# Kernel tuning notes

Measured on AMD Instinct MI355X. Metric: run time of the kernel, lower is better.

The kernel has to match this reference:

```python
import jax, jax.numpy as jnp
import numpy as np

PE_SIZE = 16          # sqrt(num_patches=256)
HIDDEN_STRIDE = 2
CUBIC_A = -0.75       # torch bicubic coefficient


def cubic_resize_matrix(in_size, out_size, a=CUBIC_A):
    """(out_size, in_size) weights for torch bicubic, align_corners=False."""
    dst = np.arange(out_size)
    src = (dst + 0.5) * in_size / out_size - 0.5
    x0 = np.floor(src).astype(np.int64)
    W = np.zeros((out_size, in_size), np.float32)
    for k in range(-1, 3):  # 4 taps
        idx = np.clip(x0 + k, 0, in_size - 1)  # border replicate
        d = np.abs(src - (x0 + k))
        w = np.where(d <= 1.0, (a + 2) * d**3 - (a + 3) * d**2 + 1.0,
            np.where(d < 2.0, a * d**3 - 5 * a * d**2 + 8 * a * d - 4 * a, 0.0))
        np.add.at(W, (dst, idx), w.astype(np.float32))
    return W


def setup_inputs() -> dict:
    key = jax.random.key(0)
    k1, k2, k3, k4 = jax.random.split(key, 4)
    n_img, t, h, w = 8, 1, 64, 64
    total = n_img * t * h * w  # 32768 patches
    in_feat, d = 3 * 14 * 14, 1152
    return {
        "pixel_values": jax.random.normal(k1, (total, in_feat), jnp.float32),
        "w_patch": jax.random.normal(k2, (d, in_feat), jnp.float32) * 0.02,
        "b_patch": jax.random.normal(k3, (d,), jnp.float32) * 0.02,
        "pos_table": jax.random.normal(k4, (PE_SIZE * PE_SIZE, d), jnp.float32) * 0.02,
        "grid_thws": jnp.array([[t, h, w]] * n_img, jnp.int64),
    }


def _pos_embed(pos_table, grid):
    """grid: np int array (n_img, 3) -> (sum t*h*w, d) positional embeddings."""
    d = pos_table.shape[-1]
    pe_grid = pos_table.reshape(PE_SIZE, PE_SIZE, d)  # (H, W, d)
    s = HIDDEN_STRIDE
    pieces = []
    for t, h, w in grid:
        Wh = jnp.asarray(cubic_resize_matrix(PE_SIZE, int(h)))
        Ww = jnp.asarray(cubic_resize_matrix(PE_SIZE, int(w)))
        pe = jnp.einsum('hH,wW,HWd->hwd', Wh, Ww, pe_grid)  # (h, w, d)
        # hidden_stride window rearrange: (h,w,d) -> (h/s, w/s, s, s, d)
        pe = pe.reshape(h // s, s, w // s, s, d).transpose(0, 2, 1, 3, 4)
        pe = pe.reshape(h * w, d)
        pe = jnp.tile(pe, (int(t), 1))  # repeat over temporal dim
        pieces.append(pe)
    return jnp.concatenate(pieces, axis=0)


def reference(pixel_values, w_patch, b_patch, pos_table, grid_thws):
    # patch embedding (Linear)
    patch_embeds = pixel_values @ w_patch.T + b_patch  # (N, d)
    grid = np.asarray(grid_thws)  # static shapes per image
    pos = _pos_embed(pos_table, grid)
    return patch_embeds + pos
```

## Files before the change

### kernel.cpp

```cpp
#include <hip/hip_runtime.h>

typedef unsigned short ushort_t;
typedef unsigned int uint_t;

typedef __bf16 bf16x8 __attribute__((ext_vector_type(8)));
typedef float f32x4 __attribute__((ext_vector_type(4)));

#define KK 588
#define KP 608
#define NN 1152
#define MM 32768
#define POSROWS 4096


__device__ __forceinline__ ushort_t f2bf(float f) {
    union { float f; uint_t u; } v; v.f = f;
    uint_t u = v.u;
    uint_t r = (u + 0x7FFFu + ((u >> 16) & 1u)) >> 16;
    return (ushort_t)r;
}

__device__ __forceinline__ void cubic_taps(int dst, float* w, int* idx) {
    const float A = -0.75f;
    float src = (float)dst * 0.25f - 0.25f;
    int x0 = (int)floorf(src);
    #pragma unroll
    for (int k = -1; k <= 2; ++k) {
        int i = x0 + k;
        int ic = i < 0 ? 0 : (i > 15 ? 15 : i);
        float d = fabsf(src - (float)i);
        float wt;
        if (d <= 1.0f)      wt = ((A + 2.0f) * d - (A + 3.0f)) * d * d + 1.0f;
        else if (d < 2.0f)  wt = ((A * d - 5.0f * A) * d + 8.0f * A) * d - 4.0f * A;
        else                wt = 0.0f;
        w[k + 1] = wt;
        idx[k + 1] = ic;
    }
}


__global__ void pos_kernel(const float* __restrict__ pt, float* __restrict__ pos) {
    int n = blockIdx.x;
    int h = ((n >> 7) << 1) | ((n >> 1) & 1);
    int w = (((n >> 2) & 31) << 1) | (n & 1);
    float wh[4], ww[4];
    int ih[4], iw[4];
    cubic_taps(h, wh, ih);
    cubic_taps(w, ww, iw);
    for (int j = threadIdx.x; j < NN; j += blockDim.x) {
        float s = 0.f;
        #pragma unroll
        for (int a = 0; a < 4; ++a) {
            float rs = 0.f;
            #pragma unroll
            for (int b = 0; b < 4; ++b)
                rs += ww[b] * pt[(ih[a] * 16 + iw[b]) * NN + j];
            s += wh[a] * rs;
        }
        pos[(size_t)n * NN + j] = s;
    }
}


__global__ void cvt_pad_kernel(const float* __restrict__ src, ushort_t* __restrict__ dst,
                               int rows) {
    int idx = blockIdx.x * 256 + threadIdx.x;
    int total = rows * KP;
    if (idx >= total) return;
    int row = idx / KP;
    int k = idx - row * KP;
    float v = (k < KK) ? src[(size_t)row * KK + k] : 0.0f;
    dst[idx] = f2bf(v);
}


__global__ void gemm_kernel(const ushort_t* __restrict__ Abf,
                            const ushort_t* __restrict__ Bbf,
                            const float* __restrict__ bias,
                            const float* __restrict__ pos,
                            float* __restrict__ out) {
    __shared__ __align__(16) ushort_t lA[128 * 32];
    __shared__ __align__(16) ushort_t lB[128 * 32];

    const int t = threadIdx.x;
    const int lane = t & 63;
    const int wid = t >> 6;
    const int wm = wid >> 1, wn = wid & 1;

    const int bm = (int)blockIdx.x * 128;
    const int bn = (int)blockIdx.y * 128;

    f32x4 acc[4][4] = {};

    for (int ks = 0; ks < KP / 32; ++ks) {
        const int k0 = ks * 32;
        #pragma unroll
        for (int i = 0; i < 2; ++i) {
            int idx = i * 256 + t;
            int row = idx >> 2;
            int slot = idx & 3;
            int khi = slot ^ ((row >> 1) & 3);
            const ushort_t* gA = Abf + (size_t)(bm + row) * KP + k0 + khi * 8;
            const ushort_t* gB = Bbf + (size_t)(bn + row) * KP + k0 + khi * 8;
            ushort_t* lAp = lA + (size_t)(idx & ~63) * 8;
            ushort_t* lBp = lB + (size_t)(idx & ~63) * 8;
            __builtin_amdgcn_global_load_lds(
                (const __attribute__((address_space(1))) void*)gA,
                (__attribute__((address_space(3))) void*)lAp, 16, 0, 0);
            __builtin_amdgcn_global_load_lds(
                (const __attribute__((address_space(1))) void*)gB,
                (__attribute__((address_space(3))) void*)lBp, 16, 0, 0);
        }
        __syncthreads();

        bf16x8 af[4], bfr[4];
        #pragma unroll
        for (int mi = 0; mi < 4; ++mi) {
            int row = wm * 64 + mi * 16 + (lane & 15);
            int slot = (lane >> 4) ^ ((row >> 1) & 3);
            af[mi] = *(const bf16x8*)(lA + row * 32 + slot * 8);
        }
        #pragma unroll
        for (int ni = 0; ni < 4; ++ni) {
            int row = wn * 64 + ni * 16 + (lane & 15);
            int slot = (lane >> 4) ^ ((row >> 1) & 3);
            bfr[ni] = *(const bf16x8*)(lB + row * 32 + slot * 8);
        }
        #pragma unroll
        for (int mi = 0; mi < 4; ++mi)
            #pragma unroll
            for (int ni = 0; ni < 4; ++ni)
                acc[mi][ni] = __builtin_amdgcn_mfma_f32_16x16x32_bf16(
                    af[mi], bfr[ni], acc[mi][ni], 0, 0, 0);
        __syncthreads();
    }

    #pragma unroll
    for (int mi = 0; mi < 4; ++mi) {
        #pragma unroll
        for (int ni = 0; ni < 4; ++ni) {
            int col = bn + wn * 64 + ni * 16 + (lane & 15);
            float bcol = bias[col];
            #pragma unroll
            for (int r = 0; r < 4; ++r) {
                int row = bm + wm * 64 + mi * 16 + (lane >> 4) * 4 + r;
                int prow = row & (POSROWS - 1);
                out[(size_t)row * NN + col] =
                    acc[mi][ni][r] + bcol + pos[(size_t)prow * NN + col];
            }
        }
    }
}


__global__ void fb_kernel(const float* __restrict__ A, const float* __restrict__ W,
                          const float* __restrict__ bias, const float* __restrict__ pt,
                          float* __restrict__ out) {
    __shared__ float sA[16][17], sB[16][17];
    int ty = threadIdx.y, tx = threadIdx.x;
    int row = blockIdx.y * 16 + ty;
    int col = blockIdx.x * 16 + tx;
    float acc = 0.f;
    for (int k0 = 0; k0 < KK; k0 += 16) {
        int ka = k0 + tx;
        sA[ty][tx] = (ka < KK) ? A[(size_t)row * KK + ka] : 0.f;
        sB[ty][tx] = (ka < KK) ? W[(size_t)(blockIdx.x * 16 + ty) * KK + ka] : 0.f;
        __syncthreads();
        #pragma unroll
        for (int kk = 0; kk < 16; ++kk)
            acc += sA[ty][kk] * sB[tx][kk];
        __syncthreads();
    }
    int n = row & (POSROWS - 1);
    int h = ((n >> 7) << 1) | ((n >> 1) & 1);
    int w = (((n >> 2) & 31) << 1) | (n & 1);
    float wh[4], ww[4]; int ih[4], iw[4];
    cubic_taps(h, wh, ih);
    cubic_taps(w, ww, iw);
    float p = 0.f;
    #pragma unroll
    for (int a = 0; a < 4; ++a) {
        float rs = 0.f;
        #pragma unroll
        for (int b = 0; b < 4; ++b)
            rs += ww[b] * pt[(ih[a] * 16 + iw[b]) * NN + col];
        p += wh[a] * rs;
    }
    out[(size_t)row * NN + col] = acc + bias[col] + p;
}


extern "C" void kernel_launch(void* const* d_in, const int* in_sizes, int n_in,
                              void* d_out, int out_size, void* d_ws, size_t ws_size,
                              hipStream_t stream) {
    const float* pv   = (const float*)d_in[0];
    const float* wp   = (const float*)d_in[1];
    const float* bias = (const float*)d_in[2];
    const float* pt   = (const float*)d_in[3];
    float* out = (float*)d_out;

    const size_t pos_bytes = (size_t)POSROWS * NN * 4;
    const size_t pvb_bytes = (size_t)MM * KP * 2;
    const size_t wb_bytes  = (size_t)NN * KP * 2;
    const size_t need = pos_bytes + pvb_bytes + wb_bytes;

    if (ws_size >= need) {
        float* pos = (float*)d_ws;
        ushort_t* pvb = (ushort_t*)((char*)d_ws + pos_bytes);
        ushort_t* wb  = (ushort_t*)((char*)d_ws + pos_bytes + pvb_bytes);

        pos_kernel<<<POSROWS, 256, 0, stream>>>(pt, pos);

        int tot_pv = MM * KP;
        cvt_pad_kernel<<<(tot_pv + 255) / 256, 256, 0, stream>>>(pv, pvb, MM);
        int tot_w = NN * KP;
        cvt_pad_kernel<<<(tot_w + 255) / 256, 256, 0, stream>>>(wp, wb, NN);

        gemm_kernel<<<dim3(MM / 128, NN / 128), 256, 0, stream>>>(pvb, wb, bias, pos, out);
    } else {
        fb_kernel<<<dim3(NN / 16, MM / 16), dim3(16, 16), 0, stream>>>(pv, wp, bias, pt, out);
    }
}
```

Measured before the change: 141.6 us.

## Triple-buffer GEMM loads, remap tiles per XCD, vectorize pos and conversion kernels

The GEMM now keeps three LDS buffers and prefetches two K-steps ahead, using explicit vmcnt waits and raw barriers so global-to-LDS loads overlap the MFMA work. Workgroups are remapped to a 1D grid so that consecutive tiles land on the same XCD for L2 reuse. The pos kernel uses float4 loads with one thread per four columns, and the fp32-to-bf16 pad conversion handles 8 elements per thread with vector loads and stores. This costs three times the LDS per block, which may lower occupancy, and the hand-written wait counts depend on exactly four loads being issued per stage.

Measured after the change: 131.9 us. -6.9%, faster.

```diff
diff --git a/kernel.cpp b/kernel.cpp
--- a/kernel.cpp
+++ b/kernel.cpp
@@ -11,14 +11,10 @@
 #define NN 1152
 #define MM 32768
 #define POSROWS 4096
-
-
-__device__ __forceinline__ ushort_t f2bf(float f) {
-    union { float f; uint_t u; } v; v.f = f;
-    uint_t u = v.u;
-    uint_t r = (u + 0x7FFFu + ((u >> 16) & 1u)) >> 16;
-    return (ushort_t)r;
-}
+#define NSTEP 19
+#define GRID 2304
+#define CHUNKS_PER_ROW 76
+
 
 __device__ __forceinline__ void cubic_taps(int dst, float* w, int* idx) {
     const float A = -0.75f;
@@ -47,30 +43,42 @@
     int ih[4], iw[4];
     cubic_taps(h, wh, ih);
     cubic_taps(w, ww, iw);
-    for (int j = threadIdx.x; j < NN; j += blockDim.x) {
-        float s = 0.f;
-        #pragma unroll
-        for (int a = 0; a < 4; ++a) {
-            float rs = 0.f;
-            #pragma unroll
-            for (int b = 0; b < 4; ++b)
-                rs += ww[b] * pt[(ih[a] * 16 + iw[b]) * NN + j];
-            s += wh[a] * rs;
-        }
-        pos[(size_t)n * NN + j] = s;
-    }
+    int tid = threadIdx.x;
+    if (tid >= NN / 4) return;
+    const f32x4* pt4 = (const f32x4*)pt;
+    f32x4 s = {0.f, 0.f, 0.f, 0.f};
+    #pragma unroll
+    for (int a = 0; a < 4; ++a) {
+        #pragma unroll
+        for (int b = 0; b < 4; ++b) {
+            float wt = wh[a] * ww[b];
+            f32x4 v = pt4[(ih[a] * 16 + iw[b]) * (NN / 4) + tid];
+            s.x += wt * v.x; s.y += wt * v.y; s.z += wt * v.z; s.w += wt * v.w;
+        }
+    }
+    ((f32x4*)pos)[(size_t)n * (NN / 4) + tid] = s;
 }
 
 
 __global__ void cvt_pad_kernel(const float* __restrict__ src, ushort_t* __restrict__ dst,
                                int rows) {
-    int idx = blockIdx.x * 256 + threadIdx.x;
-    int total = rows * KP;
-    if (idx >= total) return;
-    int row = idx / KP;
-    int k = idx - row * KP;
-    float v = (k < KK) ? src[(size_t)row * KK + k] : 0.0f;
-    dst[idx] = f2bf(v);
+    int c = blockIdx.x * 256 + threadIdx.x;
+    if (c >= rows * CHUNKS_PER_ROW) return;
+    int row = c / CHUNKS_PER_ROW;
+    int k0 = (c - row * CHUNKS_PER_ROW) * 8;
+    const float* g = src + (size_t)row * KK + k0;
+    bf16x8 v;
+    if (k0 + 8 <= KK) {
+        f32x4 a = *(const f32x4*)g;
+        f32x4 b = *(const f32x4*)(g + 4);
+        #pragma unroll
+        for (int e = 0; e < 4; ++e) { v[e] = (__bf16)a[e]; v[e + 4] = (__bf16)b[e]; }
+    } else {
+        #pragma unroll
+        for (int e = 0; e < 8; ++e)
+            v[e] = (k0 + e < KK) ? (__bf16)g[e] : (__bf16)0.f;
+    }
+    *(bf16x8*)(dst + (size_t)row * KP + k0) = v;
 }
 
 
@@ -79,31 +87,37 @@
                             const float* __restrict__ bias,
                             const float* __restrict__ pos,
                             float* __restrict__ out) {
-    __shared__ __align__(16) ushort_t lA[128 * 32];
-    __shared__ __align__(16) ushort_t lB[128 * 32];
+    __shared__ __align__(16) ushort_t lA[3][128 * 32];
+    __shared__ __align__(16) ushort_t lB[3][128 * 32];
 
     const int t = threadIdx.x;
     const int lane = t & 63;
     const int wid = t >> 6;
     const int wm = wid >> 1, wn = wid & 1;
 
-    const int bm = (int)blockIdx.x * 128;
-    const int bn = (int)blockIdx.y * 128;
+    int linear = (int)blockIdx.x;
+    int xcd = linear & 7;
+    int local = linear >> 3;
+    int wg = xcd * (GRID / 8) + local;
+    int mt = wg / 9;
+    int nt = wg - mt * 9;
+    const int bm = mt * 128;
+    const int bn = nt * 128;
 
     f32x4 acc[4][4] = {};
 
-    for (int ks = 0; ks < KP / 32; ++ks) {
+    auto stage = [&](int ks, int buf) {
         const int k0 = ks * 32;
         #pragma unroll
-        for (int i = 0; i < 2; ++i) {
-            int idx = i * 256 + t;
+        for (int j = 0; j < 2; ++j) {
+            int idx = j * 256 + t;
             int row = idx >> 2;
             int slot = idx & 3;
             int khi = slot ^ ((row >> 1) & 3);
             const ushort_t* gA = Abf + (size_t)(bm + row) * KP + k0 + khi * 8;
             const ushort_t* gB = Bbf + (size_t)(bn + row) * KP + k0 + khi * 8;
-            ushort_t* lAp = lA + (size_t)(idx & ~63) * 8;
-            ushort_t* lBp = lB + (size_t)(idx & ~63) * 8;
+            ushort_t* lAp = &lA[buf][(size_t)(idx & ~63) * 8];
+            ushort_t* lBp = &lB[buf][(size_t)(idx & ~63) * 8];
             __builtin_amdgcn_global_load_lds(
                 (const __attribute__((address_space(1))) void*)gA,
                 (__attribute__((address_space(3))) void*)lAp, 16, 0, 0);
@@ -111,20 +125,37 @@
                 (const __attribute__((address_space(1))) void*)gB,
                 (__attribute__((address_space(3))) void*)lBp, 16, 0, 0);
         }
-        __syncthreads();
+    };
+
+    stage(0, 0);
+    stage(1, 1);
+
+    for (int ks = 0; ks < NSTEP; ++ks) {
+        const int cur = ks % 3;
+
+        if (ks + 2 < NSTEP) {
+            stage(ks + 2, (ks + 2) % 3);
+            asm volatile("s_waitcnt vmcnt(8)" ::: "memory");
+        } else if (ks + 1 < NSTEP) {
+            asm volatile("s_waitcnt vmcnt(4)" ::: "memory");
+        } else {
+            asm volatile("s_waitcnt vmcnt(0)" ::: "memory");
+        }
+        __builtin_amdgcn_s_barrier();
+        __builtin_amdgcn_sched_barrier(0);
 
         bf16x8 af[4], bfr[4];
         #pragma unroll
         for (int mi = 0; mi < 4; ++mi) {
             int row = wm * 64 + mi * 16 + (lane & 15);
             int slot = (lane >> 4) ^ ((row >> 1) & 3);
-            af[mi] = *(const bf16x8*)(lA + row * 32 + slot * 8);
+            af[mi] = *(const bf16x8*)(&lA[cur][row * 32 + slot * 8]);
         }
         #pragma unroll
         for (int ni = 0; ni < 4; ++ni) {
             int row = wn * 64 + ni * 16 + (lane & 15);
             int slot = (lane >> 4) ^ ((row >> 1) & 3);
-            bfr[ni] = *(const bf16x8*)(lB + row * 32 + slot * 8);
+            bfr[ni] = *(const bf16x8*)(&lB[cur][row * 32 + slot * 8]);
         }
         #pragma unroll
         for (int mi = 0; mi < 4; ++mi)
@@ -132,7 +163,9 @@
             for (int ni = 0; ni < 4; ++ni)
                 acc[mi][ni] = __builtin_amdgcn_mfma_f32_16x16x32_bf16(
                     af[mi], bfr[ni], acc[mi][ni], 0, 0, 0);
-        __syncthreads();
+
+        asm volatile("s_waitcnt lgkmcnt(0)" ::: "memory");
+        __builtin_amdgcn_s_barrier();
     }
 
     #pragma unroll
@@ -209,14 +242,14 @@
         ushort_t* pvb = (ushort_t*)((char*)d_ws + pos_bytes);
         ushort_t* wb  = (ushort_t*)((char*)d_ws + pos_bytes + pvb_bytes);
 
-        pos_kernel<<<POSROWS, 256, 0, stream>>>(pt, pos);
-
-        int tot_pv = MM * KP;
-        cvt_pad_kernel<<<(tot_pv + 255) / 256, 256, 0, stream>>>(pv, pvb, MM);
-        int tot_w = NN * KP;
-        cvt_pad_kernel<<<(tot_w + 255) / 256, 256, 0, stream>>>(wp, wb, NN);
-
-        gemm_kernel<<<dim3(MM / 128, NN / 128), 256, 0, stream>>>(pvb, wb, bias, pos, out);
+        pos_kernel<<<POSROWS, 320, 0, stream>>>(pt, pos);
+
+        int ca = MM * CHUNKS_PER_ROW;
+        cvt_pad_kernel<<<(ca + 255) / 256, 256, 0, stream>>>(pv, pvb, MM);
+        int cb = NN * CHUNKS_PER_ROW;
+        cvt_pad_kernel<<<(cb + 255) / 256, 256, 0, stream>>>(wp, wb, NN);
+
+        gemm_kernel<<<GRID, 256, 0, stream>>>(pvb, wb, bias, pos, out);
     } else {
         fb_kernel<<<dim3(NN / 16, MM / 16), dim3(16, 16), 0, stream>>>(pv, wp, bias, pt, out);
     }
```
